# Optimization experiments

Hardware: AMD Instinct MI355X
Metric: run time of the kernel (lower is better)

## Reference

```python
import jax, jax.numpy as jnp
import numpy as np

B, S, HID = 2, 2048, 2048
H = 16
HD = HID // H            # 128
HD2 = HD // 2            # 64 (rope dim per head)
LAT = HID // 8           # 256 latent dim
BASE = 10000.0


def _rotary_table(seq_len):
    # inv_freq over rope dim HD2
    inv_freq = 1.0 / (BASE ** (jnp.arange(0, HD2, 2, dtype=jnp.float32) / HD2))  # [HD2//2]
    pos = jnp.arange(seq_len, dtype=jnp.float32)
    sincos = pos[:, None] * inv_freq[None, :]                 # [S, HD2//2]
    return jnp.concatenate([jnp.sin(sincos), jnp.cos(sincos)], axis=-1)  # [S, HD2]


def _apply_rope(x, emb):
    # x: [B, S, H, HD2]; emb: [S, HD2]
    half = HD2 // 2
    x1, x2 = x[..., :half], x[..., half:]
    sin = emb[None, :, None, :half]
    cos = emb[None, :, None, half:]
    return jnp.concatenate([x1 * cos - x2 * sin, x1 * sin + x2 * cos], axis=-1)


def setup_inputs() -> dict:
    key = jax.random.key(0)
    ks = jax.random.split(key, 9)
    s = 0.02
    return {
        "hidden_states": jax.random.normal(ks[0], (B, S, HID), jnp.float32),
        "w_kv_d": jax.random.normal(ks[1], (HID, LAT), jnp.float32) * s,
        "w_q_d": jax.random.normal(ks[2], (HID, LAT), jnp.float32) * s,
        "w_k_u": jax.random.normal(ks[3], (LAT, H * HD2), jnp.float32) * s,
        "w_q_u": jax.random.normal(ks[4], (LAT, H * HD2), jnp.float32) * s,
        "w_v_u": jax.random.normal(ks[5], (LAT, H * HD), jnp.float32) * s,
        "w_rope_k": jax.random.normal(ks[6], (HID, HID // 2), jnp.float32) * s,
        "w_rope_q": jax.random.normal(ks[7], (LAT, HID // 2), jnp.float32) * s,
        "w_o": jax.random.normal(ks[8], (HID, HID), jnp.float32) * s,
    }


def reference(hidden_states, w_kv_d, w_q_d, w_k_u, w_q_u, w_v_u, w_rope_k, w_rope_q, w_o):
    b, s, _ = hidden_states.shape
    kv_d = hidden_states @ w_kv_d            # [B,S,LAT]
    q_d = hidden_states @ w_q_d              # [B,S,LAT]
    k_p = (kv_d @ w_k_u).reshape(b, s, H, HD2)
    q_p = (q_d @ w_q_u).reshape(b, s, H, HD2)
    v = (kv_d @ w_v_u).reshape(b, s, H, HD)
    k_r = (hidden_states @ w_rope_k).reshape(b, s, H, HD2)
    q_r = (q_d @ w_rope_q).reshape(b, s, H, HD2)

    emb = _rotary_table(s)
    k_r = _apply_rope(k_r, emb)
    q_r = _apply_rope(q_r, emb)

    k = jnp.concatenate([k_p, k_r], axis=-1)  # [B,S,H,HD]
    q = jnp.concatenate([q_p, q_r], axis=-1)

    scores = jnp.einsum('bqhd,bkhd->bhqk', q, k) / jnp.sqrt(jnp.float32(HD))
    causal = jnp.tril(jnp.ones((s, s), dtype=bool))
    scores = jnp.where(causal[None, None], scores, jnp.float32(-1e9))
    probs = jax.nn.softmax(scores, axis=-1)
    out = jnp.einsum('bhqk,bkhd->bqhd', probs, v).reshape(b, s, HID)
    return out @ w_o
```

## Files before the change

kernel.cpp:

```cpp
#include <hip/hip_runtime.h>
#include <hip/hip_bf16.h>

#define BB 2
#define SS 2048
#define HID 2048
#define NH 16
#define BS (BB*SS)
#define SCALE 0.088388347648318447f
#define C2LOG 0.12751743f

typedef __bf16 bf16x8 __attribute__((ext_vector_type(8)));
typedef float f32x4 __attribute__((ext_vector_type(4)));
typedef float f32x16 __attribute__((ext_vector_type(16)));
typedef unsigned int uintx2 __attribute__((ext_vector_type(2)));

__device__ __forceinline__ bf16x8 ld_frag(const __hip_bfloat16* p) {
    uint4 u = *reinterpret_cast<const uint4*>(p);
    return __builtin_bit_cast(bf16x8, u);
}
__device__ __forceinline__ void store_c(__hip_bfloat16* C, size_t idx, float v) {
    C[idx] = __float2bfloat16(v);
}
__device__ __forceinline__ void store_c(float* C, size_t idx, float v) {
    C[idx] = v;
}
__device__ __forceinline__ ushort bf_bits(float v) {
    __hip_bfloat16 h = __float2bfloat16(v);
    return *reinterpret_cast<ushort*>(&h);
}

#define GLD16(gp, lp) \
  __builtin_amdgcn_global_load_lds((const __attribute__((address_space(1))) void*)(gp), \
                                   (__attribute__((address_space(3))) void*)(lp), 16, 0, 0)

__global__ __launch_bounds__(256) void convert_kernel(
    const float* __restrict__ src, __hip_bfloat16* __restrict__ dst, int n8)
{
    int i = blockIdx.x * blockDim.x + threadIdx.x;
    if (i >= n8) return;
    float4 a = reinterpret_cast<const float4*>(src)[2 * i];
    float4 b = reinterpret_cast<const float4*>(src)[2 * i + 1];
    ushort u[8] = { bf_bits(a.x), bf_bits(a.y), bf_bits(a.z), bf_bits(a.w),
                    bf_bits(b.x), bf_bits(b.y), bf_bits(b.z), bf_bits(b.w) };
    reinterpret_cast<uint4*>(dst)[i] = *reinterpret_cast<uint4*>(u);
}

__global__ __launch_bounds__(256) void transpose_weights_kernel(
    const float* s0, const float* s1, const float* s2, const float* s3,
    const float* s4, const float* s5, const float* s6, const float* s7,
    __hip_bfloat16* WT1, __hip_bfloat16* WT2, __hip_bfloat16* WT3,
    __hip_bfloat16* WTo)
{
    const float* srcs[8] = { s0, s1, s2, s3, s4, s5, s6, s7 };
    const int Rs[8] = { 2048, 2048, 2048, 256, 256, 256, 256, 2048 };
    const int Cs[8] = { 256, 256, 1024, 1024, 2048, 1024, 1024, 2048 };
    __hip_bfloat16* dsts[8] = {
        WT1, WT1 + (size_t)256 * 2048, WT1 + (size_t)512 * 2048,
        WT2, WT2 + (size_t)1024 * 256,
        WT3, WT3 + (size_t)1024 * 256,
        WTo };
    const int prefix[9] = { 0, 512, 1024, 3072, 3328, 3840, 4096, 4352, 8448 };

    int bid = blockIdx.x;
    int seg = 0;
    #pragma unroll
    for (int i = 0; i < 8; i++) if (bid >= prefix[i + 1]) seg = i + 1;
    int local = bid - prefix[seg];
    int R = Rs[seg], C = Cs[seg];
    int tilesC = C / 32;
    int tr = local / tilesC, tc = local % tilesC;
    int r0 = tr * 32, c0 = tc * 32;
    const float* src = srcs[seg];
    __hip_bfloat16* dst = dsts[seg];

    __shared__ float Ts[32][33];
    int t = threadIdx.x;
    int ty = t >> 5, tx = t & 31;
    #pragma unroll
    for (int k = 0; k < 4; k++) {
        int r = ty + k * 8;
        Ts[r][tx] = src[(size_t)(r0 + r) * C + c0 + tx];
    }
    __syncthreads();
    #pragma unroll
    for (int k = 0; k < 4; k++) {
        int r = ty + k * 8;
        dst[(size_t)(c0 + r) * R + r0 + tx] = __float2bfloat16(Ts[tx][r]);
    }
}

template <typename TC>
__global__ __launch_bounds__(256) void gemm_bt_kernel(
    const __hip_bfloat16* __restrict__ A, int lda,
    const __hip_bfloat16* __restrict__ Bt,
    TC* __restrict__ C0, int ldc0, int sp0, int off0, float cm0,
    TC* __restrict__ C1, int ldc1, int sp1, int off1, float cm1,
    int splitN, int K)
{
    __shared__ alignas(16) __hip_bfloat16 As[128 * 32];
    __shared__ alignas(16) __hip_bfloat16 Bs[128 * 32];

    const int nwg = gridDim.x * gridDim.y;
    int lin = blockIdx.y * gridDim.x + blockIdx.x;
    lin = (lin & 7) * (nwg >> 3) + (lin >> 3);
    const int bn = (lin % gridDim.x) * 128;
    const int bm = (lin / gridDim.x) * 128;

    const int t = threadIdx.x;
    const int w = t >> 6;
    const int lane = t & 63;
    const int l15 = lane & 15;
    const int quad = lane >> 4;
    const int wm = (w & 1) * 64;
    const int wn = (w >> 1) * 64;

    const int srow = lane >> 2;
    const int skcol = (lane & 3) * 8;

    f32x4 acc[4][4] = {};

    for (int k0 = 0; k0 < K; k0 += 32) {
        __syncthreads();
        #pragma unroll
        for (int i = 0; i < 2; i++) {
            int r = w * 32 + i * 16 + srow;
            GLD16(A + (size_t)(bm + r) * lda + k0 + skcol, &As[r * 32 + skcol]);
            GLD16(Bt + (size_t)(bn + r) * K + k0 + skcol, &Bs[r * 32 + skcol]);
        }
        __syncthreads();

        bf16x8 af[4], bf[4];
        #pragma unroll
        for (int mt = 0; mt < 4; mt++)
            af[mt] = ld_frag(&As[(wm + mt * 16 + l15) * 32 + quad * 8]);
        #pragma unroll
        for (int nt = 0; nt < 4; nt++)
            bf[nt] = ld_frag(&Bs[(wn + nt * 16 + l15) * 32 + quad * 8]);
        #pragma unroll
        for (int mt = 0; mt < 4; mt++)
            #pragma unroll
            for (int nt = 0; nt < 4; nt++)
                acc[mt][nt] = __builtin_amdgcn_mfma_f32_16x16x32_bf16(
                    af[mt], bf[nt], acc[mt][nt], 0, 0, 0);
    }

    #pragma unroll
    for (int nt = 0; nt < 4; nt++) {
        int col = bn + wn + nt * 16 + l15;
        TC* Cp; int c, ld, s64, off; float cm;
        if (col < splitN) { Cp = C0; c = col; ld = ldc0; s64 = sp0; off = off0; cm = cm0; }
        else { Cp = C1; c = col - splitN; ld = ldc1; s64 = sp1; off = off1; cm = cm1; }
        if (s64 == 2) {
            #pragma unroll
            for (int mt = 0; mt < 4; mt++) {
                int row0 = bm + wm + mt * 16 + quad * 4;
                #pragma unroll
                for (int r = 0; r < 4; r++)
                    store_c(Cp, (size_t)c * 4096 + row0 + r, acc[mt][nt][r] * cm);
            }
        } else {
            int oc = s64 ? ((c >> 6) * 128 + (c & 63) + off) : c;
            #pragma unroll
            for (int mt = 0; mt < 4; mt++) {
                #pragma unroll
                for (int r = 0; r < 4; r++) {
                    int row = bm + wm + mt * 16 + quad * 4 + r;
                    store_c(Cp, (size_t)row * ld + oc, acc[mt][nt][r] * cm);
                }
            }
        }
    }
}

__global__ __launch_bounds__(256) void rope_kernel(
    __hip_bfloat16* __restrict__ Kb, __hip_bfloat16* __restrict__ Qb)
{
    int idx = blockIdx.x * blockDim.x + threadIdx.x;
    if (idx >= BS * NH * 32) return;
    int i = idx & 31;
    int h = (idx >> 5) & 15;
    int row = idx >> 9;
    int s = row & (SS - 1);

    float inv = exp2f(-(float)i * 0.4152410118609203f);
    float ang = (float)s * inv;
    float sn = sinf(ang), cs = cosf(ang);

    size_t obase = (size_t)row * 2048 + h * 128 + 64 + i;
    {
        float x1 = __bfloat162float(Kb[obase]);
        float x2 = __bfloat162float(Kb[obase + 32]);
        Kb[obase]      = __float2bfloat16(x1 * cs - x2 * sn);
        Kb[obase + 32] = __float2bfloat16(x1 * sn + x2 * cs);
    }
    {
        float x1 = __bfloat162float(Qb[obase]);
        float x2 = __bfloat162float(Qb[obase + 32]);
        Qb[obase]      = __float2bfloat16(x1 * cs - x2 * sn);
        Qb[obase + 32] = __float2bfloat16(x1 * sn + x2 * cs);
    }
}

__global__ __launch_bounds__(512) void flash_attn_kernel(
    const __hip_bfloat16* __restrict__ Q,
    const __hip_bfloat16* __restrict__ Kb,
    const __hip_bfloat16* __restrict__ Vt,
    __hip_bfloat16* __restrict__ O)
{
    __shared__ alignas(16) __hip_bfloat16 Ktd[2 * 16 * 512];
    __shared__ alignas(16) __hip_bfloat16 Vsd[2 * 16 * 512];

    const int p = blockIdx.x;
    const int h = blockIdx.y;
    const int b = blockIdx.z;
    const int t = threadIdx.x;
    const int w = t >> 6;
    const int lane = t & 63;
    const int l31 = lane & 31;
    const int hi = lane >> 5;

    const int qt = (w < 4) ? (15 - p) : p;
    const int wq = w & 3;
    const int qwb = qt * 128 + wq * 32;
    const int q = qwb + l31;
    const int my_nt = 2 * qt + 1 + (wq >> 1);
    const int nbig = 2 * (15 - p) + 2;

    const __hip_bfloat16* Kbase = Kb + (size_t)(b * SS) * 2048 + h * 128;
    const __hip_bfloat16* Vtb = Vt + (size_t)(h * 128) * 4096 + b * SS;

    bf16x8 qf[8];
    {
        const __hip_bfloat16* qrow = Q + (size_t)(b * SS + q) * 2048 + h * 128;
        #pragma unroll
        for (int s = 0; s < 8; s++)
            qf[s] = ld_frag(qrow + s * 16 + hi * 8);
    }

    const int kb_w = w >> 2, ks0 = (2 * w) & 7;
    const int dt_w = w >> 1, vs0 = (2 * w) & 3;
    const size_t kg_l = (size_t)l31 * 2048 + hi * 8;
    const size_t vg_l = (size_t)(dt_w * 32 + l31) * 4096 + hi * 8;
    const int loff = lane * 8;

    float m_i = -INFINITY;
    float l_i = 0.0f;
    f32x16 acc[4] = {};

    #pragma unroll
    for (int i = 0; i < 2; i++)
        GLD16(Kbase + (size_t)(kb_w * 32) * 2048 + kg_l + (ks0 + i) * 16,
              &Ktd[(kb_w * 8 + ks0 + i) * 512 + loff]);
    #pragma unroll
    for (int i = 0; i < 2; i++)
        GLD16(Vtb + vg_l + (vs0 + i) * 16,
              &Vsd[(dt_w * 4 + vs0 + i) * 512 + loff]);
    asm volatile("" :: "v"(qf[0]), "v"(qf[1]), "v"(qf[2]), "v"(qf[3]),
                       "v"(qf[4]), "v"(qf[5]), "v"(qf[6]), "v"(qf[7]));

    for (int kt = 0; kt < nbig; kt++) {
        const int kvb = kt * 64;
        const int par = kt & 1;
        const bool active = (kt < my_nt);

        __builtin_amdgcn_s_barrier();
        asm volatile("" ::: "memory");

        {
            const int kvb1 = ((kt + 1 < nbig) ? kt + 1 : kt) * 64;
            const int pn = (par ^ 1) * 8192;
            #pragma unroll
            for (int i = 0; i < 2; i++)
                GLD16(Kbase + (size_t)(kvb1 + kb_w * 32) * 2048 + kg_l + (ks0 + i) * 16,
                      &Ktd[pn + (kb_w * 8 + ks0 + i) * 512 + loff]);
            #pragma unroll
            for (int i = 0; i < 2; i++)
                GLD16(Vtb + vg_l + kvb1 + (vs0 + i) * 16,
                      &Vsd[pn + (dt_w * 4 + vs0 + i) * 512 + loff]);
        }
        asm volatile("s_waitcnt vmcnt(4)" ::: "memory");
        __builtin_amdgcn_s_barrier();
        asm volatile("" ::: "memory");

        if (active) {
            const __hip_bfloat16* kb_base = &Ktd[par * 8192];
            const __hip_bfloat16* vb_base = &Vsd[par * 8192];

            f32x16 st[2] = {};
            __builtin_amdgcn_s_setprio(1);
            #pragma unroll
            for (int s = 0; s < 8; s++)
                #pragma unroll
                for (int kb = 0; kb < 2; kb++) {
                    bf16x8 kf = ld_frag(kb_base + (kb * 8 + s) * 512 + loff);
                    st[kb] = __builtin_amdgcn_mfma_f32_32x32x16_bf16(
                        kf, qf[s], st[kb], 0, 0, 0);
                }
            __builtin_amdgcn_s_setprio(0);

            float tmx = -INFINITY;
            if (kvb + 63 > qwb) {
                const int thr = q - kvb - 4 * hi;
                #pragma unroll
                for (int kb = 0; kb < 2; kb++)
                    #pragma unroll
                    for (int g = 0; g < 4; g++)
                        #pragma unroll
                        for (int r = 0; r < 4; r++) {
                            const int e = g * 4 + r;
                            float v = (kb * 32 + 8 * g + r <= thr) ? st[kb][e] : -INFINITY;
                            st[kb][e] = v;
                            tmx = fmaxf(tmx, v);
                        }
            } else {
                #pragma unroll
                for (int kb = 0; kb < 2; kb++)
                    #pragma unroll
                    for (int e = 0; e < 16; e++)
                        tmx = fmaxf(tmx, st[kb][e]);
            }
            tmx = fmaxf(tmx, __shfl_xor(tmx, 32));
            const float m2x = tmx * C2LOG;

            const bool nosc = __all(m2x <= m_i + 8.0f);
            const float mnew = nosc ? m_i : fmaxf(m_i, m2x);
            float rs = 0.0f;
            #pragma unroll
            for (int kb = 0; kb < 2; kb++)
                #pragma unroll
                for (int e = 0; e < 16; e++) {
                    float pv = exp2f(fmaf(st[kb][e], C2LOG, -mnew));
                    st[kb][e] = pv;
                    rs += pv;
                }
            rs += __shfl_xor(rs, 32);
            if (!nosc) {
                const float alpha = exp2f(m_i - mnew);
                m_i = mnew;
                l_i *= alpha;
                #pragma unroll
                for (int dt = 0; dt < 4; dt++)
                    #pragma unroll
                    for (int e = 0; e < 16; e++)
                        acc[dt][e] *= alpha;
            }
            l_i += rs;

            uint4 af[4];
            #pragma unroll
            for (int kb = 0; kb < 2; kb++) {
                unsigned int pk[4][2];
                #pragma unroll
                for (int g = 0; g < 4; g++)
                    #pragma unroll
                    for (int i = 0; i < 2; i++) {
                        float2 fp = make_float2(st[kb][g * 4 + 2 * i],
                                                st[kb][g * 4 + 2 * i + 1]);
                        __hip_bfloat162 h2 = __float22bfloat162_rn(fp);
                        pk[g][i] = *reinterpret_cast<unsigned int*>(&h2);
                    }
                #pragma unroll
                for (int sl = 0; sl < 2; sl++) {
                    uintx2 r0 = __builtin_amdgcn_permlane32_swap(
                        pk[2 * sl][0], pk[2 * sl + 1][0], false, false);
                    uintx2 r1 = __builtin_amdgcn_permlane32_swap(
                        pk[2 * sl][1], pk[2 * sl + 1][1], false, false);
                    af[kb * 2 + sl] = make_uint4(r0[0], r1[0], r0[1], r1[1]);
                }
            }

            __builtin_amdgcn_s_setprio(1);
            #pragma unroll
            for (int s = 0; s < 4; s++) {
                bf16x8 pf = __builtin_bit_cast(bf16x8, af[s]);
                #pragma unroll
                for (int dt = 0; dt < 4; dt++) {
                    bf16x8 vf = ld_frag(vb_base + (dt * 4 + s) * 512 + loff);
                    acc[dt] = __builtin_amdgcn_mfma_f32_32x32x16_bf16(
                        vf, pf, acc[dt], 0, 0, 0);
                }
            }
            __builtin_amdgcn_s_setprio(0);
        }
    }

    const float inv_l = 1.0f / l_i;
    __hip_bfloat16* orow = O + (size_t)(b * SS + q) * 2048 + h * 128;
    #pragma unroll
    for (int dt = 0; dt < 4; dt++)
        #pragma unroll
        for (int g = 0; g < 4; g++) {
            ushort u[4];
            #pragma unroll
            for (int r = 0; r < 4; r++)
                u[r] = bf_bits(acc[dt][g * 4 + r] * inv_l);
            *reinterpret_cast<uint2*>(orow + dt * 32 + 8 * g + 4 * hi) =
                *reinterpret_cast<uint2*>(u);
        }
}

extern "C" void kernel_launch(void* const* d_in, const int* in_sizes, int n_in,
                              void* d_out, int out_size, void* d_ws, size_t ws_size,
                              hipStream_t stream)
{
    const float* hs       = (const float*)d_in[0];
    const float* w_kv_d   = (const float*)d_in[1];
    const float* w_q_d    = (const float*)d_in[2];
    const float* w_k_u    = (const float*)d_in[3];
    const float* w_q_u    = (const float*)d_in[4];
    const float* w_v_u    = (const float*)d_in[5];
    const float* w_rope_k = (const float*)d_in[6];
    const float* w_rope_q = (const float*)d_in[7];
    const float* w_o      = (const float*)d_in[8];
    float* out = (float*)d_out;

    char* p = (char*)d_ws;
    auto alloc = [&](size_t nelem) {
        __hip_bfloat16* r = (__hip_bfloat16*)p;
        p += nelem * sizeof(__hip_bfloat16);
        return r;
    };
    __hip_bfloat16* hsb  = alloc((size_t)BS * HID);
    __hip_bfloat16* qkvd = alloc((size_t)BS * 512);
    __hip_bfloat16* WT1  = alloc((size_t)1536 * 2048);
    __hip_bfloat16* WT2  = alloc((size_t)3072 * 256);
    __hip_bfloat16* WT3  = alloc((size_t)2048 * 256);
    __hip_bfloat16* WTo  = alloc((size_t)2048 * 2048);
    __hip_bfloat16* Kbuf = alloc((size_t)BS * HID);
    __hip_bfloat16* Qbuf = alloc((size_t)BS * HID);
    __hip_bfloat16* Vtb  = alloc((size_t)HID * BS);
    __hip_bfloat16* attn = hsb;

    dim3 blk(256);

    convert_kernel<<<dim3((BS * HID / 8 + 255) / 256), blk, 0, stream>>>(
        hs, hsb, BS * HID / 8);
    transpose_weights_kernel<<<dim3(8448), blk, 0, stream>>>(
        w_kv_d, w_q_d, w_rope_k, w_k_u, w_v_u, w_q_u, w_rope_q, w_o,
        WT1, WT2, WT3, WTo);

    gemm_bt_kernel<__hip_bfloat16><<<dim3(1536 / 128, BS / 128), blk, 0, stream>>>(
        hsb, 2048, WT1,
        qkvd, 512, 0, 0, 1.0f,
        Kbuf, 2048, 1, 64, 1.0f,
        512, 2048);
    gemm_bt_kernel<__hip_bfloat16><<<dim3(3072 / 128, BS / 128), blk, 0, stream>>>(
        qkvd, 512, WT2,
        Kbuf, 2048, 1, 0, 1.0f,
        Vtb, 0, 2, 0, 1.0f,
        1024, 256);
    gemm_bt_kernel<__hip_bfloat16><<<dim3(2048 / 128, BS / 128), blk, 0, stream>>>(
        qkvd + 256, 512, WT3,
        Qbuf, 2048, 1, 0, 1.0f,
        Qbuf, 2048, 1, 64, 1.0f,
        1024, 256);
    rope_kernel<<<dim3((BS * NH * 32 + 255) / 256), blk, 0, stream>>>(Kbuf, Qbuf);
    flash_attn_kernel<<<dim3(8, NH, BB), dim3(512), 0, stream>>>(
        Qbuf, Kbuf, Vtb, attn);
    gemm_bt_kernel<float><<<dim3(2048 / 128, BS / 128), blk, 0, stream>>>(
        attn, 2048, WTo,
        out, 2048, 0, 0, 1.0f,
        out, 2048, 0, 0, 1.0f,
        2048, 2048);
}
```

Baseline: 351.3 us.

## Store K and V in fragment-ordered per-head layout for contiguous attention tile loads

```diff
diff --git a/kernel.cpp b/kernel.cpp
--- a/kernel.cpp
+++ b/kernel.cpp
@@ -32,6 +32,7 @@
 #define GLD16(gp, lp) \
   __builtin_amdgcn_global_load_lds((const __attribute__((address_space(1))) void*)(gp), \
                                    (__attribute__((address_space(3))) void*)(lp), 16, 0, 0)
+
 
 __global__ __launch_bounds__(256) void convert_kernel(
     const float* __restrict__ src, __hip_bfloat16* __restrict__ dst, int n8)
@@ -158,6 +159,38 @@
                 for (int r = 0; r < 4; r++)
                     store_c(Cp, (size_t)c * 4096 + row0 + r, acc[mt][nt][r] * cm);
             }
+        } else if (s64 == 3) {
+            const int hh = c >> 6, d = off + (c & 63);
+            const size_t dbase = (size_t)(d >> 4) * 512
+                               + (size_t)((d >> 3) & 1) * 256 + (d & 7);
+            #pragma unroll
+            for (int mt = 0; mt < 4; mt++) {
+                #pragma unroll
+                for (int r = 0; r < 4; r++) {
+                    int m = bm + wm + mt * 16 + quad * 4 + r;
+                    int bb2 = m >> 11, kv = m & 2047;
+                    size_t idx = (size_t)(bb2 * 16 + hh) * 262144
+                               + (size_t)(kv >> 5) * 4096 + dbase
+                               + (size_t)(kv & 31) * 8;
+                    store_c(Cp, idx, acc[mt][nt][r] * cm);
+                }
+            }
+        } else if (s64 == 4) {
+            const int hh = c >> 7, d = c & 127;
+            const size_t dbase = (size_t)(d >> 5) * 2048 + (size_t)(d & 31) * 8;
+            #pragma unroll
+            for (int mt = 0; mt < 4; mt++) {
+                #pragma unroll
+                for (int r = 0; r < 4; r++) {
+                    int m = bm + wm + mt * 16 + quad * 4 + r;
+                    int bb2 = m >> 11, kv = m & 2047;
+                    size_t idx = (size_t)(bb2 * 16 + hh) * 262144
+                               + (size_t)(kv >> 6) * 8192 + dbase
+                               + (size_t)((kv >> 4) & 3) * 512
+                               + (size_t)((kv >> 3) & 1) * 256 + (kv & 7);
+                    store_c(Cp, idx, acc[mt][nt][r] * cm);
+                }
+            }
         } else {
             int oc = s64 ? ((c >> 6) * 128 + (c & 63) + off) : c;
             #pragma unroll
@@ -173,7 +206,7 @@
 }
 
 __global__ __launch_bounds__(256) void rope_kernel(
-    __hip_bfloat16* __restrict__ Kb, __hip_bfloat16* __restrict__ Qb)
+    __hip_bfloat16* __restrict__ Kf, __hip_bfloat16* __restrict__ Qb)
 {
     int idx = blockIdx.x * blockDim.x + threadIdx.x;
     if (idx >= BS * NH * 32) return;
@@ -181,19 +214,23 @@
     int h = (idx >> 5) & 15;
     int row = idx >> 9;
     int s = row & (SS - 1);
+    int b = row >> 11;
 
     float inv = exp2f(-(float)i * 0.4152410118609203f);
     float ang = (float)s * inv;
     float sn = sinf(ang), cs = cosf(ang);
 
-    size_t obase = (size_t)row * 2048 + h * 128 + 64 + i;
     {
-        float x1 = __bfloat162float(Kb[obase]);
-        float x2 = __bfloat162float(Kb[obase + 32]);
-        Kb[obase]      = __float2bfloat16(x1 * cs - x2 * sn);
-        Kb[obase + 32] = __float2bfloat16(x1 * sn + x2 * cs);
+        size_t kaddr = ((size_t)(b * 16 + h) * 64 + (s >> 5)) * 4096
+                     + (size_t)(4 + (i >> 4)) * 512
+                     + (size_t)(((i >> 3) & 1) * 32 + (s & 31)) * 8 + (i & 7);
+        float x1 = __bfloat162float(Kf[kaddr]);
+        float x2 = __bfloat162float(Kf[kaddr + 1024]);
+        Kf[kaddr]        = __float2bfloat16(x1 * cs - x2 * sn);
+        Kf[kaddr + 1024] = __float2bfloat16(x1 * sn + x2 * cs);
     }
     {
+        size_t obase = (size_t)row * 2048 + h * 128 + 64 + i;
         float x1 = __bfloat162float(Qb[obase]);
         float x2 = __bfloat162float(Qb[obase + 32]);
         Qb[obase]      = __float2bfloat16(x1 * cs - x2 * sn);
@@ -203,8 +240,8 @@
 
 __global__ __launch_bounds__(512) void flash_attn_kernel(
     const __hip_bfloat16* __restrict__ Q,
-    const __hip_bfloat16* __restrict__ Kb,
-    const __hip_bfloat16* __restrict__ Vt,
+    const __hip_bfloat16* __restrict__ Kf,
+    const __hip_bfloat16* __restrict__ Vf,
     __hip_bfloat16* __restrict__ O)
 {
     __shared__ alignas(16) __hip_bfloat16 Ktd[2 * 16 * 512];
@@ -226,8 +263,8 @@
     const int my_nt = 2 * qt + 1 + (wq >> 1);
     const int nbig = 2 * (15 - p) + 2;
 
-    const __hip_bfloat16* Kbase = Kb + (size_t)(b * SS) * 2048 + h * 128;
-    const __hip_bfloat16* Vtb = Vt + (size_t)(h * 128) * 4096 + b * SS;
+    const __hip_bfloat16* Kfb = Kf + (size_t)(b * 16 + h) * 262144;
+    const __hip_bfloat16* Vfb = Vf + (size_t)(b * 16 + h) * 262144;
 
     bf16x8 qf[8];
     {
@@ -237,10 +274,7 @@
             qf[s] = ld_frag(qrow + s * 16 + hi * 8);
     }
 
-    const int kb_w = w >> 2, ks0 = (2 * w) & 7;
-    const int dt_w = w >> 1, vs0 = (2 * w) & 3;
-    const size_t kg_l = (size_t)l31 * 2048 + hi * 8;
-    const size_t vg_l = (size_t)(dt_w * 32 + l31) * 4096 + hi * 8;
+    const int kreg = (w & 1) * 8 + (w >> 1) * 2;
     const int loff = lane * 8;
 
     float m_i = -INFINITY;
@@ -249,12 +283,11 @@
 
     #pragma unroll
     for (int i = 0; i < 2; i++)
-        GLD16(Kbase + (size_t)(kb_w * 32) * 2048 + kg_l + (ks0 + i) * 16,
-              &Ktd[(kb_w * 8 + ks0 + i) * 512 + loff]);
+        GLD16(Kfb + (size_t)(w & 1) * 4096 + ((w >> 1) * 2 + i) * 512 + loff,
+              &Ktd[(kreg + i) * 512 + loff]);
     #pragma unroll
     for (int i = 0; i < 2; i++)
-        GLD16(Vtb + vg_l + (vs0 + i) * 16,
-              &Vsd[(dt_w * 4 + vs0 + i) * 512 + loff]);
+        GLD16(Vfb + (2 * w + i) * 512 + loff, &Vsd[(2 * w + i) * 512 + loff]);
     asm volatile("" :: "v"(qf[0]), "v"(qf[1]), "v"(qf[2]), "v"(qf[3]),
                        "v"(qf[4]), "v"(qf[5]), "v"(qf[6]), "v"(qf[7]));
 
@@ -263,24 +296,24 @@
         const int par = kt & 1;
         const bool active = (kt < my_nt);
 
+        asm volatile("s_waitcnt vmcnt(0)" ::: "memory");
         __builtin_amdgcn_s_barrier();
         asm volatile("" ::: "memory");
 
         {
-            const int kvb1 = ((kt + 1 < nbig) ? kt + 1 : kt) * 64;
+            const int kt1 = (kt + 1 < nbig) ? kt + 1 : kt;
             const int pn = (par ^ 1) * 8192;
+            const size_t ksrc = (size_t)(2 * kt1 + (w & 1)) * 4096 + (w >> 1) * 1024;
             #pragma unroll
             for (int i = 0; i < 2; i++)
-                GLD16(Kbase + (size_t)(kvb1 + kb_w * 32) * 2048 + kg_l + (ks0 + i) * 16,
-                      &Ktd[pn + (kb_w * 8 + ks0 + i) * 512 + loff]);
+                GLD16(Kfb + ksrc + i * 512 + loff,
+                      &Ktd[pn + (kreg + i) * 512 + loff]);
+            const size_t vsrc = (size_t)kt1 * 8192 + 2 * w * 512;
             #pragma unroll
             for (int i = 0; i < 2; i++)
-                GLD16(Vtb + vg_l + kvb1 + (vs0 + i) * 16,
-                      &Vsd[pn + (dt_w * 4 + vs0 + i) * 512 + loff]);
+                GLD16(Vfb + vsrc + i * 512 + loff,
+                      &Vsd[pn + (2 * w + i) * 512 + loff]);
         }
-        asm volatile("s_waitcnt vmcnt(4)" ::: "memory");
-        __builtin_amdgcn_s_barrier();
-        asm volatile("" ::: "memory");
 
         if (active) {
             const __hip_bfloat16* kb_base = &Ktd[par * 8192];
@@ -426,9 +459,9 @@
     __hip_bfloat16* WT2  = alloc((size_t)3072 * 256);
     __hip_bfloat16* WT3  = alloc((size_t)2048 * 256);
     __hip_bfloat16* WTo  = alloc((size_t)2048 * 2048);
-    __hip_bfloat16* Kbuf = alloc((size_t)BS * HID);
+    __hip_bfloat16* Kf   = alloc((size_t)BS * HID);
     __hip_bfloat16* Qbuf = alloc((size_t)BS * HID);
-    __hip_bfloat16* Vtb  = alloc((size_t)HID * BS);
+    __hip_bfloat16* Vf   = alloc((size_t)HID * BS);
     __hip_bfloat16* attn = hsb;
 
     dim3 blk(256);
@@ -442,21 +475,21 @@
     gemm_bt_kernel<__hip_bfloat16><<<dim3(1536 / 128, BS / 128), blk, 0, stream>>>(
         hsb, 2048, WT1,
         qkvd, 512, 0, 0, 1.0f,
-        Kbuf, 2048, 1, 64, 1.0f,
+        Kf, 0, 3, 64, 1.0f,
         512, 2048);
     gemm_bt_kernel<__hip_bfloat16><<<dim3(3072 / 128, BS / 128), blk, 0, stream>>>(
         qkvd, 512, WT2,
-        Kbuf, 2048, 1, 0, 1.0f,
-        Vtb, 0, 2, 0, 1.0f,
+        Kf, 0, 3, 0, 1.0f,
+        Vf, 0, 4, 0, 1.0f,
         1024, 256);
     gemm_bt_kernel<__hip_bfloat16><<<dim3(2048 / 128, BS / 128), blk, 0, stream>>>(
         qkvd + 256, 512, WT3,
         Qbuf, 2048, 1, 0, 1.0f,
         Qbuf, 2048, 1, 64, 1.0f,
         1024, 256);
-    rope_kernel<<<dim3((BS * NH * 32 + 255) / 256), blk, 0, stream>>>(Kbuf, Qbuf);
+    rope_kernel<<<dim3((BS * NH * 32 + 255) / 256), blk, 0, stream>>>(Kf, Qbuf);
     flash_attn_kernel<<<dim3(8, NH, BB), dim3(512), 0, stream>>>(
-        Qbuf, Kbuf, Vtb, attn);
+        Qbuf, Kf, Vf, attn);
     gemm_bt_kernel<float><<<dim3(2048 / 128, BS / 128), blk, 0, stream>>>(
         attn, 2048, WTo,
         out, 2048, 0, 0, 1.0f,
```

Result: no change. 345.6 us (-1.6%).
